# Optimization experiments

Measured on AMD Instinct MI355X. Metric: run time of the kernel, lower is better.

## Reference

```python
import jax, jax.numpy as jnp
import numpy as np

B, S, D, H = 2, 2048, 1024, 16
MAX_DIST = 1024


def setup_inputs() -> dict:
    key = jax.random.key(0)
    ks = jax.random.split(key, 7)
    w = lambda k, shape: jax.random.normal(k, shape, jnp.float32) * 0.02
    return {
        "x": jax.random.normal(ks[0], (B, S, D), jnp.float32),
        "Wq": w(ks[1], (D, D)), "bq": jnp.zeros((D,), jnp.float32),
        "Wk": w(ks[2], (D, D)),
        "Wv": w(ks[3], (D, D)), "bv": jnp.zeros((D,), jnp.float32),
        "Wo": w(ks[4], (D, D)), "bo": jnp.zeros((D,), jnp.float32),
        "pos_bias": w(ks[5], (2 * MAX_DIST - 1, H)),
        "max_dist": MAX_DIST,
    }


def reference(x, Wq, bq, Wk, Wv, bv, Wo, bo, pos_bias, max_dist):
    b, s, d_model = x.shape
    h = pos_bias.shape[1]
    hd = d_model // h  # head dim
    scale = hd ** -0.25  # module's scale applied to (QK^T + rel_bias)

    split = lambda t: t.reshape(b, s, h, hd).transpose(0, 2, 1, 3)  # [b,h,s,hd]
    q = split(x @ Wq + bq)
    k = split(x @ Wk)          # key has no bias
    v = split(x @ Wv + bv)

    # raw QK^T (unscaled), as in the module
    scores = jnp.einsum('bhqd,bhkd->bhqk', q, k)

    # relative-position bias gather: clamp(i-j) -> table index
    pos = jnp.arange(s)[:, None] - jnp.arange(s)[None, :]
    pos = jnp.clip(pos, -max_dist + 1, max_dist - 1) + max_dist - 1
    rel_bias = pos_bias[pos].transpose(2, 0, 1)[None]  # [1,h,s,s]

    # SDPA with attn_mask = (scores + rel_bias)*scale adds it on top of QK^T/sqrt(hd)
    logits = scores * (1.0 / jnp.sqrt(jnp.float32(hd))) + (scores + rel_bias) * scale
    w = jax.nn.softmax(logits, axis=-1)

    out = jnp.einsum('bhqk,bhkd->bhqd', w, v)
    out = out.transpose(0, 2, 1, 3).reshape(b, s, d_model)
    return out @ Wo + bo
```

## Files before the change

kernel.cpp:

```cpp
#include <hip/hip_runtime.h>
#include <hip/hip_bf16.h>
#include <cstddef>
#include <cstdint>

#define BATCH   2
#define S_LEN   2048
#define D_MODEL 1024
#define NH      16
#define HD      64
#define MAXD    1024

#define SCORE_SCALE 0.47855339059327373f
#define BIAS_SCALE  0.35355339059327373f
#define FIXM 8.0f
#define LOG2E 1.4426950408889634f

typedef __attribute__((ext_vector_type(8))) short bf16x8;
typedef __attribute__((ext_vector_type(4))) short bf16x4;
typedef __attribute__((ext_vector_type(4))) float f32x4;

#if __has_builtin(__builtin_amdgcn_mfma_f32_16x16x16bf16_1k)
#define USE_1K 1
#else
#define USE_1K 0
#endif

static __device__ __forceinline__ unsigned short f2bf(float f) {
    __hip_bfloat16 h = __float2bfloat16(f);
    return *reinterpret_cast<unsigned short*>(&h);
}
static __device__ __forceinline__ float bf2f(unsigned short u) {
    union { unsigned int i; float f; } c;
    c.i = ((unsigned int)u) << 16;
    return c.f;
}

#define GLDS(gp, lp) __builtin_amdgcn_global_load_lds( \
    (const __attribute__((address_space(1))) void*)(gp), \
    (__attribute__((address_space(3))) void*)(lp), 16, 0, 0)

__global__ __launch_bounds__(256) void prep(
    const float* __restrict__ x,
    const float* __restrict__ Wq, const float* __restrict__ Wk,
    const float* __restrict__ Wv, const float* __restrict__ Wo,
    const float* __restrict__ pos_bias,
    unsigned short* __restrict__ xb, unsigned short* __restrict__ Wqkvt,
    unsigned short* __restrict__ Wot,
    float* __restrict__ pb_t)
{
    __shared__ float t[32][33];
    const int bx = blockIdx.x, tid = threadIdx.x;

    if (bx < 2048) {
        const size_t i = ((size_t)bx * 256 + tid) * 8;
        const float4 a = *(const float4*)(x + i);
        const float4 b = *(const float4*)(x + i + 4);
        unsigned short u[8] = {f2bf(a.x), f2bf(a.y), f2bf(a.z), f2bf(a.w),
                               f2bf(b.x), f2bf(b.y), f2bf(b.z), f2bf(b.w)};
        *(uint4*)(xb + i) = *(const uint4*)u;
    } else if (bx < 6144) {
        const int bx2 = bx - 2048;
        const int z = bx2 >> 10, inner = bx2 & 1023;
        const int gx = inner & 31, gy = inner >> 5;
        const float* W = (z == 0) ? Wq : (z == 1) ? Wk : (z == 2) ? Wv : Wo;
        unsigned short* hi = (z < 3) ? Wqkvt + (size_t)z * 1024 * 1024 : Wot;
        const int bxx = gx * 32, byy = gy * 32;
        const int tx = tid & 31, ty = tid >> 5;
        #pragma unroll
        for (int i = 0; i < 4; i++)
            t[ty + 8 * i][tx] = W[(size_t)(byy + ty + 8 * i) * 1024 + bxx + tx];
        __syncthreads();
        #pragma unroll
        for (int i = 0; i < 4; i++) {
            const float v = t[tx][ty + 8 * i];
            const size_t o = (size_t)(bxx + ty + 8 * i) * 1024 + byy + tx;
            hi[o] = f2bf(v);
        }
    } else {
        const int o0 = (bx - 6144) * 1024 + tid * 4;
        float v[4];
        #pragma unroll
        for (int j = 0; j < 4; j++) {
            const int o = o0 + j;
            const int hh = o >> 12, ii = o & 4095;
            int rel = ii - 2047;
            rel = min(max(rel, -(MAXD - 1)), MAXD - 1);
            v[j] = (BIAS_SCALE * pos_bias[(size_t)(rel + MAXD - 1) * NH + hh] - FIXM) * LOG2E;
        }
        *(float4*)&pb_t[o0] = *(const float4*)v;
    }
}

#define GBM 128
#define GBN 128
#define GBK 32

__global__ __launch_bounds__(256) void gemm_qkv(
    const unsigned short* __restrict__ A, const unsigned short* __restrict__ Bt,
    const float* __restrict__ bq, const float* __restrict__ bv,
    unsigned short* __restrict__ Cout)
{
    const int K = 1024;
    __shared__ __align__(16) unsigned short As[GBM][GBK];
    __shared__ __align__(16) unsigned short Bs[GBN][GBK];

    const int tid = threadIdx.x;
    const int wave = tid >> 6, lane = tid & 63;
    const int quad = lane >> 4, cl = lane & 15;
    const int wm = (wave & 1) * 64, wn = (wave >> 1) * 64;
    const int bm = blockIdx.y * GBM, bn = blockIdx.x * GBN;

    const int sr = wave * 32 + (lane >> 2);
    const int sc = (lane & 3) * 8;
    const unsigned short* aS0 = A  + (size_t)(bm + sr) * K + sc;
    const unsigned short* aS1 = aS0 + (size_t)16 * K;
    const unsigned short* bS0 = Bt + (size_t)(bn + sr) * K + sc;
    const unsigned short* bS1 = bS0 + (size_t)16 * K;
    unsigned short* aD0 = &As[wave * 32][0];
    unsigned short* aD1 = &As[wave * 32 + 16][0];
    unsigned short* bD0 = &Bs[wave * 32][0];
    unsigned short* bD1 = &Bs[wave * 32 + 16][0];

    f32x4 acc[4][4];
    #pragma unroll
    for (int mi = 0; mi < 4; mi++)
        #pragma unroll
        for (int ni = 0; ni < 4; ni++)
            #pragma unroll
            for (int r = 0; r < 4; r++) acc[mi][ni][r] = 0.f;

    for (int k0 = 0; k0 < K; k0 += GBK) {
        __syncthreads();
        GLDS(aS0, aD0); GLDS(aS1, aD1);
        GLDS(bS0, bD0); GLDS(bS1, bD1);
        aS0 += GBK; aS1 += GBK; bS0 += GBK; bS1 += GBK;
        __syncthreads();

        bf16x8 af[4], bf[4];
        #pragma unroll
        for (int mi = 0; mi < 4; mi++)
            af[mi] = *(const bf16x8*)&As[wm + mi * 16 + cl][quad * 8];
        #pragma unroll
        for (int ni = 0; ni < 4; ni++)
            bf[ni] = *(const bf16x8*)&Bs[wn + ni * 16 + cl][quad * 8];
        #pragma unroll
        for (int mi = 0; mi < 4; mi++)
            #pragma unroll
            for (int ni = 0; ni < 4; ni++)
                acc[mi][ni] = __builtin_amdgcn_mfma_f32_16x16x32_bf16(
                    af[mi], bf[ni], acc[mi][ni], 0, 0, 0);
    }

    #pragma unroll
    for (int ni = 0; ni < 4; ni++) {
        const int coln = bn + wn + ni * 16 + cl;
        const int region = coln >> 10, c = coln & 1023;
        const float bs = (region == 0) ? bq[c] : (region == 2) ? bv[c] : 0.f;
        #pragma unroll
        for (int mi = 0; mi < 4; mi++) {
            const int row0 = bm + wm + mi * 16 + quad * 4;
            if (region == 2) {
                const int hh = c >> 6, d = c & 63;
                const int bb = row0 >> 11, s0 = row0 & 2047;
                unsigned short u[4];
                #pragma unroll
                for (int r = 0; r < 4; r++) u[r] = f2bf(acc[mi][ni][r] + bs);
                unsigned short* dst = Cout + (size_t)8 * 1024 * 1024
                    + (((size_t)bb * NH + hh) * HD + d) * S_LEN + s0;
                *(uint2*)dst = *(const uint2*)u;
            } else {
                unsigned short* dst = Cout + (size_t)region * 4 * 1024 * 1024;
                #pragma unroll
                for (int r = 0; r < 4; r++)
                    dst[(size_t)(row0 + r) * 1024 + c] = f2bf(acc[mi][ni][r] + bs);
            }
        }
    }
}

#define TQB 64
#define TKB 64

__global__ __launch_bounds__(256) void attn_mfma(
    const unsigned short* __restrict__ Q, const unsigned short* __restrict__ K,
    const unsigned short* __restrict__ VT, const float* __restrict__ pb_t,
    unsigned short* __restrict__ O)
{
    const int qt = blockIdx.x, h = blockIdx.y, b = blockIdx.z;
    const int tid  = threadIdx.x;
    const int wave = tid >> 6, lane = tid & 63;
    const int quad = lane >> 4, col = lane & 15;
    const int qbase = qt * TQB;
    const int qw = qbase + wave * 16;

    __shared__ __align__(16) unsigned short Ks[TKB][HD];
    __shared__ __align__(16) unsigned short Vs[HD][TKB];
#if !USE_1K
    __shared__ __align__(16) unsigned short Ps[4][16][TKB];
#endif

    bf16x8 qf[2];
    {
        const unsigned short* qp =
            &Q[((size_t)(b * S_LEN) + qw + col) * D_MODEL + h * HD + quad * 8];
        qf[0] = *(const bf16x8*)qp;
        qf[1] = *(const bf16x8*)(qp + 32);
    }

    f32x4 accO[4];
    #pragma unroll
    for (int nb = 0; nb < 4; nb++)
        #pragma unroll
        for (int r = 0; r < 4; r++) accO[nb][r] = 0.f;
#if USE_1K
    f32x4 accL;
    #pragma unroll
    for (int r = 0; r < 4; r++) accL[r] = 0.f;
    const bf16x4 vone = {(short)16256, (short)16256, (short)16256, (short)16256};
#else
    float lsum = 0.f;
#endif

    const int s0 = tid, s1 = 256 + tid;
    const int kr0 = s0 >> 3, kj0 = (s0 & 7) ^ (kr0 & 7);
    const int kr1 = s1 >> 3, kj1 = (s1 & 7) ^ (kr1 & 7);
    const unsigned short* kS0 = K + ((size_t)(b * S_LEN) + kr0) * D_MODEL + h * HD + kj0 * 8;
    const unsigned short* kS1 = K + ((size_t)(b * S_LEN) + kr1) * D_MODEL + h * HD + kj1 * 8;
    const size_t vbase = ((size_t)(b * NH + h) * HD) * S_LEN;
    const unsigned short* vS0 = VT + vbase + (size_t)kr0 * S_LEN + kj0 * 8;
    const unsigned short* vS1 = VT + vbase + (size_t)kr1 * S_LEN + kj1 * 8;
    unsigned short* kD = &Ks[0][0] + wave * 512;
    unsigned short* vD = &Vs[0][0] + wave * 512;

    const float* pbh = pb_t + h * 4096;
    const float* pb_lane = pbh + (qbase + wave * 16 + col - quad * 4 + 2047);
    const float SC2 = SCORE_SCALE * LOG2E;
    const int jsw = col & 7;

    for (int kb = 0; kb < S_LEN; kb += TKB) {
        __syncthreads();
        GLDS(kS0, kD); GLDS(kS1, kD + 2048);
        GLDS(vS0, vD); GLDS(vS1, vD + 2048);
        kS0 += (size_t)TKB * D_MODEL; kS1 += (size_t)TKB * D_MODEL;
        vS0 += TKB; vS1 += TKB;

        float bias_r[16];
        #pragma unroll
        for (int nb = 0; nb < 4; nb++)
            #pragma unroll
            for (int r = 0; r < 4; r++)
                bias_r[nb * 4 + r] = pb_lane[-(nb * 16 + r)];

        __syncthreads();

        f32x4 accS[4];
        #pragma unroll
        for (int nb = 0; nb < 4; nb++)
            #pragma unroll
            for (int r = 0; r < 4; r++) accS[nb][r] = 0.f;
        #pragma unroll
        for (int kk = 0; kk < 2; kk++)
            #pragma unroll
            for (int nb = 0; nb < 4; nb++) {
                const bf16x8 kf = *(const bf16x8*)
                    &Ks[nb * 16 + col][((kk * 4 + quad) ^ jsw) * 8];
                accS[nb] = __builtin_amdgcn_mfma_f32_16x16x32_bf16(kf, qf[kk], accS[nb], 0, 0, 0);
            }

#if USE_1K
        bf16x4 pf[4];
#endif
        #pragma unroll
        for (int nb = 0; nb < 4; nb++) {
            float pr[4];
            #pragma unroll
            for (int r = 0; r < 4; r++)
                pr[r] = __builtin_amdgcn_exp2f(fmaf(accS[nb][r], SC2, bias_r[nb * 4 + r]));
            const __hip_bfloat162 h0 = __float22bfloat162_rn(make_float2(pr[0], pr[1]));
            const __hip_bfloat162 h1 = __float22bfloat162_rn(make_float2(pr[2], pr[3]));
            uint2 w;
            w.x = *(const unsigned int*)&h0;
            w.y = *(const unsigned int*)&h1;
#if USE_1K
            union { uint2 u; bf16x4 v; } cv;
            cv.u = w;
            pf[nb] = cv.v;
            accL = __builtin_amdgcn_mfma_f32_16x16x16bf16_1k(vone, pf[nb], accL, 0, 0, 0);
#else
            #pragma unroll
            for (int r = 0; r < 4; r++) lsum += pr[r];
            const int jp = ((nb * 2 + (quad >> 1)) ^ jsw) * 8 + (quad & 1) * 4;
            *(uint2*)&Ps[wave][col][jp] = w;
#endif
        }

#if USE_1K
        #pragma unroll
        for (int s = 0; s < 4; s++) {
            #pragma unroll
            for (int nb = 0; nb < 4; nb++) {
                const bf16x4 vf = *(const bf16x4*)
                    &Vs[nb * 16 + col][(((2 * s + (quad >> 1)) ^ jsw) * 8) + (quad & 1) * 4];
                accO[nb] = __builtin_amdgcn_mfma_f32_16x16x16bf16_1k(vf, pf[s], accO[nb], 0, 0, 0);
            }
        }
#else
        #pragma unroll
        for (int kk = 0; kk < 2; kk++) {
            const bf16x8 af = *(const bf16x8*)
                &Ps[wave][col][((kk * 4 + quad) ^ jsw) * 8];
            #pragma unroll
            for (int nb = 0; nb < 4; nb++) {
                const bf16x8 vf = *(const bf16x8*)
                    &Vs[nb * 16 + col][((kk * 4 + quad) ^ jsw) * 8];
                accO[nb] = __builtin_amdgcn_mfma_f32_16x16x32_bf16(af, vf, accO[nb], 0, 0, 0);
            }
        }
#endif
        pb_lane -= TKB;
    }

#if USE_1K
    const float inv = 1.0f / accL[0];
    const size_t row = (size_t)(b * S_LEN) + qw + col;
    #pragma unroll
    for (int nb = 0; nb < 4; nb++) {
        unsigned short u[4];
        #pragma unroll
        for (int r = 0; r < 4; r++) u[r] = f2bf(accO[nb][r] * inv);
        *(uint2*)&O[row * D_MODEL + h * HD + nb * 16 + quad * 4] = *(const uint2*)u;
    }
#else
    lsum += __shfl_xor(lsum, 16);
    lsum += __shfl_xor(lsum, 32);
    #pragma unroll
    for (int r = 0; r < 4; r++) {
        const float inv = 1.0f / __shfl(lsum, quad * 4 + r);
        const size_t row = (size_t)(b * S_LEN) + qw + quad * 4 + r;
        #pragma unroll
        for (int nb = 0; nb < 4; nb++)
            O[row * D_MODEL + h * HD + nb * 16 + col] = f2bf(accO[nb][r] * inv);
    }
#endif
}

#define OBM 64
#define OBN 128

__global__ __launch_bounds__(256) void gemm_out(
    const unsigned short* __restrict__ A, const unsigned short* __restrict__ Bt,
    const float* __restrict__ bias, float* __restrict__ Cout)
{
    const int N = 1024, Kd = 1024;
    __shared__ __align__(16) unsigned short As[OBM][GBK];
    __shared__ __align__(16) unsigned short Bs[OBN][GBK];

    const int tid = threadIdx.x;
    const int wave = tid >> 6, lane = tid & 63;
    const int quad = lane >> 4, cl = lane & 15;
    const int wm = (wave & 1) * 32, wn = (wave >> 1) * 64;
    const int bm = blockIdx.y * OBM, bn = blockIdx.x * OBN;

    const int ar = tid >> 2, ac = (tid & 3) * 8;
    const unsigned short* aS = A + (size_t)(bm + ar) * Kd + ac;
    const unsigned short* hS0 = Bt + (size_t)(bn + ar) * Kd + ac;
    const unsigned short* hS1 = hS0 + (size_t)64 * Kd;
    unsigned short* aD  = &As[0][0] + wave * 512;
    unsigned short* hD0 = &Bs[0][0] + wave * 512;
    unsigned short* hD1 = hD0 + 2048;

    f32x4 acc[2][4];
    #pragma unroll
    for (int mi = 0; mi < 2; mi++)
        #pragma unroll
        for (int ni = 0; ni < 4; ni++)
            #pragma unroll
            for (int r = 0; r < 4; r++) acc[mi][ni][r] = 0.f;

    for (int k0 = 0; k0 < Kd; k0 += GBK) {
        __syncthreads();
        GLDS(aS, aD);
        GLDS(hS0, hD0); GLDS(hS1, hD1);
        aS += GBK; hS0 += GBK; hS1 += GBK;
        __syncthreads();

        bf16x8 af[2], bh[4];
        #pragma unroll
        for (int mi = 0; mi < 2; mi++)
            af[mi] = *(const bf16x8*)&As[wm + mi * 16 + cl][quad * 8];
        #pragma unroll
        for (int ni = 0; ni < 4; ni++)
            bh[ni] = *(const bf16x8*)&Bs[wn + ni * 16 + cl][quad * 8];
        #pragma unroll
        for (int mi = 0; mi < 2; mi++)
            #pragma unroll
            for (int ni = 0; ni < 4; ni++)
                acc[mi][ni] = __builtin_amdgcn_mfma_f32_16x16x32_bf16(
                    af[mi], bh[ni], acc[mi][ni], 0, 0, 0);
    }

    #pragma unroll
    for (int ni = 0; ni < 4; ni++) {
        const int coln = bn + wn + ni * 16 + cl;
        const float bs = bias[coln];
        #pragma unroll
        for (int mi = 0; mi < 2; mi++) {
            const int row0 = bm + wm + mi * 16 + quad * 4;
            #pragma unroll
            for (int r = 0; r < 4; r++)
                Cout[(size_t)(row0 + r) * N + coln] = acc[mi][ni][r] + bs;
        }
    }
}

extern "C" void kernel_launch(void* const* d_in, const int* in_sizes, int n_in,
                              void* d_out, int out_size, void* d_ws, size_t ws_size,
                              hipStream_t stream)
{
    const float* x        = (const float*)d_in[0];
    const float* Wq       = (const float*)d_in[1];
    const float* bq       = (const float*)d_in[2];
    const float* Wk       = (const float*)d_in[3];
    const float* Wv       = (const float*)d_in[4];
    const float* bv       = (const float*)d_in[5];
    const float* Wo       = (const float*)d_in[6];
    const float* bo       = (const float*)d_in[7];
    const float* pos_bias = (const float*)d_in[8];
    float* out = (float*)d_out;

    const size_t ELEMS  = (size_t)BATCH * S_LEN * D_MODEL;
    const size_t WELEMS = (size_t)D_MODEL * D_MODEL;
    unsigned short* xb     = (unsigned short*)d_ws;
    unsigned short* Wqkvt  = xb + ELEMS;
    unsigned short* Wot    = Wqkvt + 3 * WELEMS;
    unsigned short* QKV    = Wot + WELEMS;
    unsigned short* Qb     = QKV;
    unsigned short* Kb     = Qb + ELEMS;
    unsigned short* VTb    = Kb + ELEMS;
    unsigned short* Ab     = VTb + ELEMS;
    float* pb_t            = (float*)(Ab + ELEMS);

    prep<<<6208, 256, 0, stream>>>(x, Wq, Wk, Wv, Wo, pos_bias,
                                   xb, Wqkvt, Wot, pb_t);

    gemm_qkv<<<dim3(3072 / GBN, 4096 / GBM), 256, 0, stream>>>(
        xb, Wqkvt, bq, bv, QKV);

    attn_mfma<<<dim3(S_LEN / TQB, NH, BATCH), 256, 0, stream>>>(
        Qb, Kb, VTb, pb_t, Ab);

    gemm_out<<<dim3(1024 / OBN, 4096 / OBM), 256, 0, stream>>>(
        Ab, Wot, bo, out);
}
```

Baseline: 211.6 us.

## Double-buffer K/V shared tiles and prefetch next tile during compute

Doubles the K and V shared-memory tiles and issues the global-to-LDS loads and bias reads for the next key block before computing on the current one. This overlaps memory latency with MFMA and exp work and cuts the two barriers per iteration to one. In exchange it doubles LDS use for K/V, which may reduce occupancy, and keeps extra bias registers live.

```diff
diff --git a/kernel.cpp b/kernel.cpp
--- a/kernel.cpp
+++ b/kernel.cpp
@@ -193,8 +193,8 @@
     const int qbase = qt * TQB;
     const int qw = qbase + wave * 16;
 
-    __shared__ __align__(16) unsigned short Ks[TKB][HD];
-    __shared__ __align__(16) unsigned short Vs[HD][TKB];
+    __shared__ __align__(16) unsigned short Ks[2][TKB][HD];
+    __shared__ __align__(16) unsigned short Vs[2][HD][TKB];
 #if !USE_1K
     __shared__ __align__(16) unsigned short Ps[4][16][TKB];
 #endif
@@ -229,29 +229,49 @@
     const size_t vbase = ((size_t)(b * NH + h) * HD) * S_LEN;
     const unsigned short* vS0 = VT + vbase + (size_t)kr0 * S_LEN + kj0 * 8;
     const unsigned short* vS1 = VT + vbase + (size_t)kr1 * S_LEN + kj1 * 8;
-    unsigned short* kD = &Ks[0][0] + wave * 512;
-    unsigned short* vD = &Vs[0][0] + wave * 512;
+    unsigned short* kD = &Ks[0][0][0] + wave * 512;
+    unsigned short* vD = &Vs[0][0][0] + wave * 512;
 
     const float* pbh = pb_t + h * 4096;
     const float* pb_lane = pbh + (qbase + wave * 16 + col - quad * 4 + 2047);
     const float SC2 = SCORE_SCALE * LOG2E;
     const int jsw = col & 7;
 
-    for (int kb = 0; kb < S_LEN; kb += TKB) {
-        __syncthreads();
-        GLDS(kS0, kD); GLDS(kS1, kD + 2048);
-        GLDS(vS0, vD); GLDS(vS1, vD + 2048);
-        kS0 += (size_t)TKB * D_MODEL; kS1 += (size_t)TKB * D_MODEL;
-        vS0 += TKB; vS1 += TKB;
-
-        float bias_r[16];
-        #pragma unroll
-        for (int nb = 0; nb < 4; nb++)
-            #pragma unroll
-            for (int r = 0; r < 4; r++)
-                bias_r[nb * 4 + r] = pb_lane[-(nb * 16 + r)];
-
-        __syncthreads();
+    GLDS(kS0, kD); GLDS(kS1, kD + 2048);
+    GLDS(vS0, vD); GLDS(vS1, vD + 2048);
+    kS0 += (size_t)TKB * D_MODEL; kS1 += (size_t)TKB * D_MODEL;
+    vS0 += TKB; vS1 += TKB;
+
+    float bias_c[16];
+    #pragma unroll
+    for (int nb = 0; nb < 4; nb++)
+        #pragma unroll
+        for (int r = 0; r < 4; r++)
+            bias_c[nb * 4 + r] = pb_lane[-(nb * 16 + r)];
+    pb_lane -= TKB;
+
+    __syncthreads();
+
+    const int NT = S_LEN / TKB;
+    #pragma unroll 2
+    for (int t = 0; t < NT; ++t) {
+        const int cur = t & 1;
+        const int curoff = cur * (TKB * HD);
+        const int nxtoff = curoff ^ (TKB * HD);
+
+        float bias_n[16];
+        if (t != NT - 1) {
+            GLDS(kS0, kD + nxtoff); GLDS(kS1, kD + nxtoff + 2048);
+            GLDS(vS0, vD + nxtoff); GLDS(vS1, vD + nxtoff + 2048);
+            kS0 += (size_t)TKB * D_MODEL; kS1 += (size_t)TKB * D_MODEL;
+            vS0 += TKB; vS1 += TKB;
+            #pragma unroll
+            for (int nb = 0; nb < 4; nb++)
+                #pragma unroll
+                for (int r = 0; r < 4; r++)
+                    bias_n[nb * 4 + r] = pb_lane[-(nb * 16 + r)];
+            pb_lane -= TKB;
+        }
 
         f32x4 accS[4];
         #pragma unroll
@@ -263,7 +283,7 @@
             #pragma unroll
             for (int nb = 0; nb < 4; nb++) {
                 const bf16x8 kf = *(const bf16x8*)
-                    &Ks[nb * 16 + col][((kk * 4 + quad) ^ jsw) * 8];
+                    &Ks[cur][nb * 16 + col][((kk * 4 + quad) ^ jsw) * 8];
                 accS[nb] = __builtin_amdgcn_mfma_f32_16x16x32_bf16(kf, qf[kk], accS[nb], 0, 0, 0);
             }
 
@@ -275,7 +295,7 @@
             float pr[4];
             #pragma unroll
             for (int r = 0; r < 4; r++)
-                pr[r] = __builtin_amdgcn_exp2f(fmaf(accS[nb][r], SC2, bias_r[nb * 4 + r]));
+                pr[r] = __builtin_amdgcn_exp2f(fmaf(accS[nb][r], SC2, bias_c[nb * 4 + r]));
             const __hip_bfloat162 h0 = __float22bfloat162_rn(make_float2(pr[0], pr[1]));
             const __hip_bfloat162 h1 = __float22bfloat162_rn(make_float2(pr[2], pr[3]));
             uint2 w;
@@ -300,7 +320,7 @@
             #pragma unroll
             for (int nb = 0; nb < 4; nb++) {
                 const bf16x4 vf = *(const bf16x4*)
-                    &Vs[nb * 16 + col][(((2 * s + (quad >> 1)) ^ jsw) * 8) + (quad & 1) * 4];
+                    &Vs[cur][nb * 16 + col][(((2 * s + (quad >> 1)) ^ jsw) * 8) + (quad & 1) * 4];
                 accO[nb] = __builtin_amdgcn_mfma_f32_16x16x16bf16_1k(vf, pf[s], accO[nb], 0, 0, 0);
             }
         }
@@ -312,12 +332,18 @@
             #pragma unroll
             for (int nb = 0; nb < 4; nb++) {
                 const bf16x8 vf = *(const bf16x8*)
-                    &Vs[nb * 16 + col][((kk * 4 + quad) ^ jsw) * 8];
+                    &Vs[cur][nb * 16 + col][((kk * 4 + quad) ^ jsw) * 8];
                 accO[nb] = __builtin_amdgcn_mfma_f32_16x16x32_bf16(af, vf, accO[nb], 0, 0, 0);
             }
         }
 #endif
-        pb_lane -= TKB;
+
+        if (t != NT - 1) {
+            #pragma unroll
+            for (int r = 0; r < 16; r++) bias_c[r] = bias_n[r];
+        }
+
+        __syncthreads();
     }
 
 #if USE_1K
```

Result: no change. 207.7 us (-1.8%).

## Double-buffer K/V tiles and process two query fragments per wave in attention

Applied to the files above, without the earlier changes.

The attention kernel now handles 128 queries per block, with each wave owning two 16-row query fragments. Each K/V fragment loaded from LDS is reused across two MFMAs, which halves K/V global and LDS traffic per query. K/V tiles and bias values are double-buffered: the next tile is prefetched via global_load_lds while the current one is computed, and there is one barrier per tile instead of two. The non-1K fallback path is removed. In exchange the kernel uses more registers and LDS, and launches half as many blocks (512), which may lower occupancy.

```diff
diff --git a/kernel.cpp b/kernel.cpp
--- a/kernel.cpp
+++ b/kernel.cpp
@@ -19,20 +19,9 @@
 typedef __attribute__((ext_vector_type(4))) short bf16x4;
 typedef __attribute__((ext_vector_type(4))) float f32x4;
 
-#if __has_builtin(__builtin_amdgcn_mfma_f32_16x16x16bf16_1k)
-#define USE_1K 1
-#else
-#define USE_1K 0
-#endif
-
 static __device__ __forceinline__ unsigned short f2bf(float f) {
     __hip_bfloat16 h = __float2bfloat16(f);
     return *reinterpret_cast<unsigned short*>(&h);
-}
-static __device__ __forceinline__ float bf2f(unsigned short u) {
-    union { unsigned int i; float f; } c;
-    c.i = ((unsigned int)u) << 16;
-    return c.f;
 }
 
 #define GLDS(gp, lp) __builtin_amdgcn_global_load_lds( \
@@ -178,7 +167,7 @@
     }
 }
 
-#define TQB 64
+#define TQB 128
 #define TKB 64
 
 __global__ __launch_bounds__(256) void attn_mfma(
@@ -191,35 +180,33 @@
     const int wave = tid >> 6, lane = tid & 63;
     const int quad = lane >> 4, col = lane & 15;
     const int qbase = qt * TQB;
-    const int qw = qbase + wave * 16;
-
-    __shared__ __align__(16) unsigned short Ks[TKB][HD];
-    __shared__ __align__(16) unsigned short Vs[HD][TKB];
-#if !USE_1K
-    __shared__ __align__(16) unsigned short Ps[4][16][TKB];
-#endif
-
-    bf16x8 qf[2];
-    {
+    const int qw = qbase + wave * 32;
+
+    __shared__ __align__(16) unsigned short Ks[2][TKB][HD];
+    __shared__ __align__(16) unsigned short Vs[2][HD][TKB];
+
+    bf16x8 qf[2][2];
+    #pragma unroll
+    for (int f = 0; f < 2; f++) {
         const unsigned short* qp =
-            &Q[((size_t)(b * S_LEN) + qw + col) * D_MODEL + h * HD + quad * 8];
-        qf[0] = *(const bf16x8*)qp;
-        qf[1] = *(const bf16x8*)(qp + 32);
-    }
-
-    f32x4 accO[4];
-    #pragma unroll
-    for (int nb = 0; nb < 4; nb++)
-        #pragma unroll
-        for (int r = 0; r < 4; r++) accO[nb][r] = 0.f;
-#if USE_1K
-    f32x4 accL;
-    #pragma unroll
-    for (int r = 0; r < 4; r++) accL[r] = 0.f;
+            &Q[((size_t)(b * S_LEN) + qw + f * 16 + col) * D_MODEL + h * HD + quad * 8];
+        qf[f][0] = *(const bf16x8*)qp;
+        qf[f][1] = *(const bf16x8*)(qp + 32);
+    }
+
+    f32x4 accO[2][4];
+    #pragma unroll
+    for (int f = 0; f < 2; f++)
+        #pragma unroll
+        for (int nb = 0; nb < 4; nb++)
+            #pragma unroll
+            for (int r = 0; r < 4; r++) accO[f][nb][r] = 0.f;
+    f32x4 accL[2];
+    #pragma unroll
+    for (int f = 0; f < 2; f++)
+        #pragma unroll
+        for (int r = 0; r < 4; r++) accL[f][r] = 0.f;
     const bf16x4 vone = {(short)16256, (short)16256, (short)16256, (short)16256};
-#else
-    float lsum = 0.f;
-#endif
 
     const int s0 = tid, s1 = 256 + tid;
     const int kr0 = s0 >> 3, kj0 = (s0 & 7) ^ (kr0 & 7);
@@ -229,119 +216,120 @@
     const size_t vbase = ((size_t)(b * NH + h) * HD) * S_LEN;
     const unsigned short* vS0 = VT + vbase + (size_t)kr0 * S_LEN + kj0 * 8;
     const unsigned short* vS1 = VT + vbase + (size_t)kr1 * S_LEN + kj1 * 8;
-    unsigned short* kD = &Ks[0][0] + wave * 512;
-    unsigned short* vD = &Vs[0][0] + wave * 512;
+    unsigned short* kD = &Ks[0][0][0] + wave * 512;
+    unsigned short* vD = &Vs[0][0][0] + wave * 512;
 
     const float* pbh = pb_t + h * 4096;
-    const float* pb_lane = pbh + (qbase + wave * 16 + col - quad * 4 + 2047);
+    const float* pb_lane = pbh + (qw + col - quad * 4 + 2047);
     const float SC2 = SCORE_SCALE * LOG2E;
     const int jsw = col & 7;
 
-    for (int kb = 0; kb < S_LEN; kb += TKB) {
-        __syncthreads();
-        GLDS(kS0, kD); GLDS(kS1, kD + 2048);
-        GLDS(vS0, vD); GLDS(vS1, vD + 2048);
-        kS0 += (size_t)TKB * D_MODEL; kS1 += (size_t)TKB * D_MODEL;
-        vS0 += TKB; vS1 += TKB;
-
-        float bias_r[16];
+    GLDS(kS0, kD); GLDS(kS1, kD + 2048);
+    GLDS(vS0, vD); GLDS(vS1, vD + 2048);
+    kS0 += (size_t)TKB * D_MODEL; kS1 += (size_t)TKB * D_MODEL;
+    vS0 += TKB; vS1 += TKB;
+
+    float biasA[2][16], biasB[2][16];
+    #pragma unroll
+    for (int f = 0; f < 2; f++)
         #pragma unroll
         for (int nb = 0; nb < 4; nb++)
             #pragma unroll
             for (int r = 0; r < 4; r++)
-                bias_r[nb * 4 + r] = pb_lane[-(nb * 16 + r)];
-
-        __syncthreads();
-
-        f32x4 accS[4];
-        #pragma unroll
-        for (int nb = 0; nb < 4; nb++)
-            #pragma unroll
-            for (int r = 0; r < 4; r++) accS[nb][r] = 0.f;
-        #pragma unroll
-        for (int kk = 0; kk < 2; kk++)
-            #pragma unroll
-            for (int nb = 0; nb < 4; nb++) {
-                const bf16x8 kf = *(const bf16x8*)
-                    &Ks[nb * 16 + col][((kk * 4 + quad) ^ jsw) * 8];
-                accS[nb] = __builtin_amdgcn_mfma_f32_16x16x32_bf16(kf, qf[kk], accS[nb], 0, 0, 0);
-            }
-
-#if USE_1K
-        bf16x4 pf[4];
-#endif
+                biasA[f][nb * 4 + r] = pb_lane[f * 16 - (nb * 16 + r)];
+    pb_lane -= TKB;
+
+    __syncthreads();
+
+    const int NT = S_LEN / TKB;
+
+#define ATT_TILE(T, P, BC, BN)                                                \
+  {                                                                           \
+    if ((T) != NT - 1) {                                                      \
+      GLDS(kS0, kD + ((P) ^ 1) * 4096); GLDS(kS1, kD + ((P) ^ 1) * 4096 + 2048); \
+      GLDS(vS0, vD + ((P) ^ 1) * 4096); GLDS(vS1, vD + ((P) ^ 1) * 4096 + 2048); \
+      kS0 += (size_t)TKB * D_MODEL; kS1 += (size_t)TKB * D_MODEL;             \
+      vS0 += TKB; vS1 += TKB;                                                 \
+      _Pragma("unroll")                                                       \
+      for (int f = 0; f < 2; f++)                                             \
+        _Pragma("unroll")                                                     \
+        for (int nb = 0; nb < 4; nb++)                                        \
+          _Pragma("unroll")                                                   \
+          for (int r = 0; r < 4; r++)                                         \
+            BN[f][nb * 4 + r] = pb_lane[f * 16 - (nb * 16 + r)];              \
+      pb_lane -= TKB;                                                         \
+    }                                                                         \
+    f32x4 accS[2][4];                                                         \
+    _Pragma("unroll")                                                         \
+    for (int f = 0; f < 2; f++)                                               \
+      _Pragma("unroll")                                                       \
+      for (int nb = 0; nb < 4; nb++)                                          \
+        _Pragma("unroll")                                                     \
+        for (int r = 0; r < 4; r++) accS[f][nb][r] = 0.f;                     \
+    _Pragma("unroll")                                                         \
+    for (int kk = 0; kk < 2; kk++)                                            \
+      _Pragma("unroll")                                                       \
+      for (int nb = 0; nb < 4; nb++) {                                        \
+        const bf16x8 kf = *(const bf16x8*)                                    \
+            &Ks[P][nb * 16 + col][((kk * 4 + quad) ^ jsw) * 8];               \
+        accS[0][nb] = __builtin_amdgcn_mfma_f32_16x16x32_bf16(                \
+            kf, qf[0][kk], accS[0][nb], 0, 0, 0);                             \
+        accS[1][nb] = __builtin_amdgcn_mfma_f32_16x16x32_bf16(                \
+            kf, qf[1][kk], accS[1][nb], 0, 0, 0);                             \
+      }                                                                       \
+    bf16x4 pf[2][4];                                                          \
+    _Pragma("unroll")                                                         \
+    for (int f = 0; f < 2; f++)                                               \
+      _Pragma("unroll")                                                       \
+      for (int nb = 0; nb < 4; nb++) {                                        \
+        float pr[4];                                                          \
+        _Pragma("unroll")                                                     \
+        for (int r = 0; r < 4; r++)                                           \
+          pr[r] = __builtin_amdgcn_exp2f(                                     \
+              fmaf(accS[f][nb][r], SC2, BC[f][nb * 4 + r]));                  \
+        const __hip_bfloat162 h0 = __float22bfloat162_rn(make_float2(pr[0], pr[1])); \
+        const __hip_bfloat162 h1 = __float22bfloat162_rn(make_float2(pr[2], pr[3])); \
+        uint2 w;                                                              \
+        w.x = *(const unsigned int*)&h0;                                      \
+        w.y = *(const unsigned int*)&h1;                                      \
+        union { uint2 u; bf16x4 v; } cv;                                      \
+        cv.u = w;                                                             \
+        pf[f][nb] = cv.v;                                                     \
+        accL[f] = __builtin_amdgcn_mfma_f32_16x16x16bf16_1k(                  \
+            vone, pf[f][nb], accL[f], 0, 0, 0);                               \
+      }                                                                       \
+    _Pragma("unroll")                                                         \
+    for (int s = 0; s < 4; s++)                                               \
+      _Pragma("unroll")                                                       \
+      for (int nb = 0; nb < 4; nb++) {                                        \
+        const bf16x4 vf = *(const bf16x4*)                                    \
+            &Vs[P][nb * 16 + col][(((2 * s + (quad >> 1)) ^ jsw) * 8) + (quad & 1) * 4]; \
+        accO[0][nb] = __builtin_amdgcn_mfma_f32_16x16x16bf16_1k(              \
+            vf, pf[0][s], accO[0][nb], 0, 0, 0);                              \
+        accO[1][nb] = __builtin_amdgcn_mfma_f32_16x16x16bf16_1k(              \
+            vf, pf[1][s], accO[1][nb], 0, 0, 0);                              \
+      }                                                                       \
+    __syncthreads();                                                          \
+  }
+
+    for (int t = 0; t < NT; t += 2) {
+        ATT_TILE(t,     0, biasA, biasB);
+        ATT_TILE(t + 1, 1, biasB, biasA);
+    }
+#undef ATT_TILE
+
+    #pragma unroll
+    for (int f = 0; f < 2; f++) {
+        const float inv = 1.0f / accL[f][0];
+        const size_t row = (size_t)(b * S_LEN) + qw + f * 16 + col;
         #pragma unroll
         for (int nb = 0; nb < 4; nb++) {
-            float pr[4];
-            #pragma unroll
-            for (int r = 0; r < 4; r++)
-                pr[r] = __builtin_amdgcn_exp2f(fmaf(accS[nb][r], SC2, bias_r[nb * 4 + r]));
-            const __hip_bfloat162 h0 = __float22bfloat162_rn(make_float2(pr[0], pr[1]));
-            const __hip_bfloat162 h1 = __float22bfloat162_rn(make_float2(pr[2], pr[3]));
-            uint2 w;
-            w.x = *(const unsigned int*)&h0;
-            w.y = *(const unsigned int*)&h1;
-#if USE_1K
-            union { uint2 u; bf16x4 v; } cv;
-            cv.u = w;
-            pf[nb] = cv.v;
-            accL = __builtin_amdgcn_mfma_f32_16x16x16bf16_1k(vone, pf[nb], accL, 0, 0, 0);
-#else
-            #pragma unroll
-            for (int r = 0; r < 4; r++) lsum += pr[r];
-            const int jp = ((nb * 2 + (quad >> 1)) ^ jsw) * 8 + (quad & 1) * 4;
-            *(uint2*)&Ps[wave][col][jp] = w;
-#endif
+            unsigned short u[4];
+            #pragma unroll
+            for (int r = 0; r < 4; r++) u[r] = f2bf(accO[f][nb][r] * inv);
+            *(uint2*)&O[row * D_MODEL + h * HD + nb * 16 + quad * 4] = *(const uint2*)u;
         }
-
-#if USE_1K
-        #pragma unroll
-        for (int s = 0; s < 4; s++) {
-            #pragma unroll
-            for (int nb = 0; nb < 4; nb++) {
-                const bf16x4 vf = *(const bf16x4*)
-                    &Vs[nb * 16 + col][(((2 * s + (quad >> 1)) ^ jsw) * 8) + (quad & 1) * 4];
-                accO[nb] = __builtin_amdgcn_mfma_f32_16x16x16bf16_1k(vf, pf[s], accO[nb], 0, 0, 0);
-            }
-        }
-#else
-        #pragma unroll
-        for (int kk = 0; kk < 2; kk++) {
-            const bf16x8 af = *(const bf16x8*)
-                &Ps[wave][col][((kk * 4 + quad) ^ jsw) * 8];
-            #pragma unroll
-            for (int nb = 0; nb < 4; nb++) {
-                const bf16x8 vf = *(const bf16x8*)
-                    &Vs[nb * 16 + col][((kk * 4 + quad) ^ jsw) * 8];
-                accO[nb] = __builtin_amdgcn_mfma_f32_16x16x32_bf16(af, vf, accO[nb], 0, 0, 0);
-            }
-        }
-#endif
-        pb_lane -= TKB;
-    }
-
-#if USE_1K
-    const float inv = 1.0f / accL[0];
-    const size_t row = (size_t)(b * S_LEN) + qw + col;
-    #pragma unroll
-    for (int nb = 0; nb < 4; nb++) {
-        unsigned short u[4];
-        #pragma unroll
-        for (int r = 0; r < 4; r++) u[r] = f2bf(accO[nb][r] * inv);
-        *(uint2*)&O[row * D_MODEL + h * HD + nb * 16 + quad * 4] = *(const uint2*)u;
-    }
-#else
-    lsum += __shfl_xor(lsum, 16);
-    lsum += __shfl_xor(lsum, 32);
-    #pragma unroll
-    for (int r = 0; r < 4; r++) {
-        const float inv = 1.0f / __shfl(lsum, quad * 4 + r);
-        const size_t row = (size_t)(b * S_LEN) + qw + quad * 4 + r;
-        #pragma unroll
-        for (int nb = 0; nb < 4; nb++)
-            O[row * D_MODEL + h * HD + nb * 16 + col] = f2bf(accO[nb][r] * inv);
-    }
-#endif
+    }
 }
 
 #define OBM 64
```

New measurement: 208.0 us. Within noise of the previous version (-1.7%).
